# Performance work log

Measured on AMD Instinct MI355X. Metric: run time of the kernel, lower is better.

## Reference

```python
import jax, jax.numpy as jnp
import numpy as np

B, L, D_MODEL = 2, 2048, 1024
N_HEADS, D_K = 16, 64  # d_v == d_k (required by the output*q epilogue)


def setup_inputs() -> dict:
    key = jax.random.key(0)
    ks = jax.random.split(key, 8)
    # xavier_normal std for [d_model, d_k] fan: sqrt(2/(d_model+d_k))
    std = float(np.sqrt(2.0 / (D_MODEL + D_K)))
    std_p = float(np.sqrt(1.0 / (N_HEADS * D_K)))  # nn.Linear default ~ U(-1/sqrt(fan_in),..); normal approx ok for a baseline
    return {
        "q": jax.random.normal(ks[0], (B, L, D_MODEL), jnp.float32),
        "k": jax.random.normal(ks[1], (B, L, D_MODEL), jnp.float32),
        "v": jax.random.normal(ks[2], (B, L, D_MODEL), jnp.float32),
        "w_qs": jax.random.normal(ks[3], (N_HEADS, D_MODEL, D_K), jnp.float32) * std,
        "w_ks": jax.random.normal(ks[4], (N_HEADS, D_MODEL, D_K), jnp.float32) * std,
        "w_vs": jax.random.normal(ks[5], (N_HEADS, D_MODEL, D_K), jnp.float32) * std,
        "w_proj": jax.random.normal(ks[6], (D_MODEL, N_HEADS * D_K), jnp.float32) * std_p,
        "b_proj": jnp.zeros((D_MODEL,), jnp.float32),
    }


def reference(q, k, v, w_qs, w_ks, w_vs, w_proj, b_proj):
    # Per-head projections: [h, B, L, d_k]
    qh = jnp.einsum("bld,hdk->hblk", q, w_qs)
    kh = jnp.einsum("bld,hdk->hblk", k, w_ks)
    vh = jnp.einsum("bld,hdk->hblk", v, w_vs)
    # UNscaled attention (no 1/sqrt(d_k)), dropout is identity at eval
    attn = jax.nn.softmax(jnp.einsum("hblk,hbmk->hblm", qh, kh), axis=-1)
    # attn @ V with elementwise *q epilogue
    out = jnp.einsum("hblm,hbmk->hblk", attn, vh) * qh
    # torch.cat(torch.split(outputs, mb_size, 0), -1): heads concat on last dim
    out = out.transpose(1, 2, 0, 3).reshape(q.shape[0], q.shape[1], -1)  # [B, L, h*d_k]
    return out @ w_proj.T + b_proj
```

## Files before the change

### kernel.cpp

```cpp
#include <hip/hip_runtime.h>

#define B_ 2
#define L_ 2048
#define DM 1024
#define H_ 16
#define DK 64
#define ROWS (B_*L_)
#define BK 32
#define LDT 40

typedef _Float16 f16x8 __attribute__((ext_vector_type(8)));
typedef float    f32x4 __attribute__((ext_vector_type(4)));
typedef unsigned short us8 __attribute__((ext_vector_type(8)));
typedef unsigned short us4v __attribute__((ext_vector_type(4)));

__device__ __forceinline__ unsigned short f2h(float f) {
    _Float16 h = (_Float16)f;
    return __builtin_bit_cast(unsigned short, h);
}
__device__ __forceinline__ float h2f(unsigned short u) {
    return (float)__builtin_bit_cast(_Float16, u);
}
__device__ __forceinline__ f16x8 ld8h(const unsigned short* p) {
    return *reinterpret_cast<const f16x8*>(p);
}
__device__ __forceinline__ us8 cvt_us8(float4 a, float4 b) {
    us8 u;
    u[0] = f2h(a.x); u[1] = f2h(a.y); u[2] = f2h(a.z); u[3] = f2h(a.w);
    u[4] = f2h(b.x); u[5] = f2h(b.y); u[6] = f2h(b.z); u[7] = f2h(b.w);
    return u;
}

#define MFMA(a, b, c) __builtin_amdgcn_mfma_f32_16x16x32_f16((a), (b), (c), 0, 0, 0)

#define AS1 __attribute__((address_space(1)))
#define AS3 __attribute__((address_space(3)))
__device__ __forceinline__ void glds16(const void* g, void* l) {
    __builtin_amdgcn_global_load_lds((const AS1 unsigned int*)g,
                                     (AS3 unsigned int*)l, 16, 0, 0);
}

__global__ __launch_bounds__(256) void kcvt(
    const float* __restrict__ src, unsigned short* __restrict__ dst)
{
    size_t i = ((size_t)blockIdx.x * 256 + threadIdx.x) * 8;
    const float4* s4 = (const float4*)(src + i);
    *(us8*)(dst + i) = cvt_us8(s4[0], s4[1]);
}

__global__ __launch_bounds__(256) void kcvt3(
    const float* __restrict__ q, const float* __restrict__ k,
    const float* __restrict__ v, unsigned short* __restrict__ dst)
{
    int bx = blockIdx.x;
    int which = bx >> 11, rem = bx & 2047;
    const float* src = (which == 0) ? q : (which == 1) ? k : v;
    size_t i = ((size_t)rem * 256 + threadIdx.x) * 8;
    const float4* s4 = (const float4*)(src + i);
    *(us8*)(dst + (size_t)which * ROWS * DM + i) = cvt_us8(s4[0], s4[1]);
}

__global__ __launch_bounds__(256) void k0_transpose_w(
    const float* __restrict__ wq,
    const float* __restrict__ wk,
    const float* __restrict__ wv,
    unsigned short* __restrict__ wt)
{
    __shared__ unsigned short tile[64][65];
    int bx = blockIdx.x;
    int which = bx / (H_ * 16);
    int rem   = bx % (H_ * 16);
    int h  = rem >> 4;
    int db = (rem & 15) * 64;
    const float* src = (which == 0) ? wq : (which == 1) ? wk : wv;
    float scale = (which == 1) ? 1.44269504f : 1.0f;

    int t = threadIdx.x;
    int r = t >> 2;
    int c = (t & 3) * 16;
    const float4* sp = (const float4*)(src + ((size_t)(h * DM + db + r)) * DK + c);
    #pragma unroll
    for (int i4 = 0; i4 < 4; i4++) {
        float4 f = sp[i4];
        tile[r][c + i4 * 4 + 0] = f2h(f.x * scale);
        tile[r][c + i4 * 4 + 1] = f2h(f.y * scale);
        tile[r][c + i4 * 4 + 2] = f2h(f.z * scale);
        tile[r][c + i4 * 4 + 3] = f2h(f.w * scale);
    }
    __syncthreads();

    int n   = t >> 2;
    int d16 = (t & 3) * 16;
    __align__(16) unsigned short ov[16];
    #pragma unroll
    for (int i = 0; i < 16; i++) ov[i] = tile[d16 + i][n];
    size_t off = (((size_t)which * H_ + h) * DK + n) * DM + db + d16;
    *(us8*)(wt + off)     = *(us8*)&ov[0];
    *(us8*)(wt + off + 8) = *(us8*)&ov[8];
}

__global__ __launch_bounds__(256) void k1_proj_fp16(
    const unsigned short* __restrict__ qkvh,
    const unsigned short* __restrict__ wt,
    unsigned short* __restrict__ qh,
    unsigned short* __restrict__ kh,
    unsigned short* __restrict__ vt)
{
    __shared__ __align__(16) unsigned short sA[128 * BK];
    __shared__ __align__(16) unsigned short sB[128 * BK];

    int bx = blockIdx.x;
    int which = bx >> 8;
    int rem   = bx & 255;
    int mbase = (rem >> 3) * 128;
    int nbase = (rem & 7) * 128;

    const unsigned short* Ag = qkvh + (size_t)which * ROWS * DM;
    const unsigned short* Bg = wt + (size_t)which * DM * DM;

    int t = threadIdx.x;
    int wave = t >> 6, lane = t & 63, quad = lane >> 4, l16 = lane & 15;
    int wm = (wave >> 1) * 64, wn = (wave & 1) * 64;

    const unsigned short* gA0 = Ag + (size_t)(mbase + (t >> 2)) * DM + (t & 3) * 8;
    const unsigned short* gA1 = gA0 + (size_t)64 * DM;
    const unsigned short* gB0 = Bg + (size_t)(nbase + (t >> 2)) * DM + (t & 3) * 8;
    const unsigned short* gB1 = gB0 + (size_t)64 * DM;
    unsigned short* lA0 = &sA[(size_t)t * 8];
    unsigned short* lA1 = &sA[(size_t)(256 + t) * 8];
    unsigned short* lB0 = &sB[(size_t)t * 8];
    unsigned short* lB1 = &sB[(size_t)(256 + t) * 8];

    f32x4 acc[4][4];
    #pragma unroll
    for (int mi = 0; mi < 4; mi++)
        #pragma unroll
        for (int ni = 0; ni < 4; ni++) acc[mi][ni] = (f32x4)0.0f;

    for (int step = 0; step < 32; step++) {
        if (step) __syncthreads();
        glds16(gA0, lA0); glds16(gA1, lA1);
        glds16(gB0, lB0); glds16(gB1, lB1);
        gA0 += BK; gA1 += BK; gB0 += BK; gB1 += BK;
        __syncthreads();

        f16x8 aF[4], bF[4];
        #pragma unroll
        for (int mi = 0; mi < 4; mi++)
            aF[mi] = *(const f16x8*)&sA[(wm + mi * 16 + l16) * BK + quad * 8];
        #pragma unroll
        for (int ni = 0; ni < 4; ni++)
            bF[ni] = *(const f16x8*)&sB[(wn + ni * 16 + l16) * BK + quad * 8];
        __builtin_amdgcn_s_setprio(1);
        #pragma unroll
        for (int mi = 0; mi < 4; mi++)
            #pragma unroll
            for (int ni = 0; ni < 4; ni++)
                acc[mi][ni] = MFMA(aF[mi], bF[ni], acc[mi][ni]);
        __builtin_amdgcn_s_setprio(0);
    }

    int h = (nbase >> 6) + (wave & 1);
    if (which < 2) {
        unsigned short* OUT = ((which == 0) ? qh : kh) + (size_t)h * ROWS * DK;
        #pragma unroll
        for (int mi = 0; mi < 4; mi++)
            #pragma unroll
            for (int ni = 0; ni < 4; ni++)
                #pragma unroll
                for (int r = 0; r < 4; r++) {
                    int row = mbase + wm + mi * 16 + quad * 4 + r;
                    OUT[(size_t)row * DK + ni * 16 + l16] = f2h(acc[mi][ni][r]);
                }
    } else {
        unsigned short* OUT = vt + (size_t)h * DK * ROWS;
        #pragma unroll
        for (int mi = 0; mi < 4; mi++)
            #pragma unroll
            for (int ni = 0; ni < 4; ni++) {
                int dk   = ni * 16 + l16;
                int rowb = mbase + wm + mi * 16 + quad * 4;
                us4v pk;
                pk[0] = f2h(acc[mi][ni][0]); pk[1] = f2h(acc[mi][ni][1]);
                pk[2] = f2h(acc[mi][ni][2]); pk[3] = f2h(acc[mi][ni][3]);
                *(us4v*)(OUT + (size_t)dk * ROWS + rowb) = pk;
            }
    }
}

__global__ __launch_bounds__(256) void k1_proj_qkv(
    const float* __restrict__ q,
    const float* __restrict__ k,
    const float* __restrict__ v,
    const unsigned short* __restrict__ wt,
    unsigned short* __restrict__ qh,
    unsigned short* __restrict__ kh,
    unsigned short* __restrict__ vt)
{
    __shared__ __align__(16) unsigned short sA[128 * LDT];
    __shared__ __align__(16) unsigned short sB[128 * LDT];

    int bx = blockIdx.x;
    int which = bx >> 8;
    int rem   = bx & 255;
    int mbase = (rem >> 3) * 128;
    int nbase = (rem & 7) * 128;

    const float* Ag = (which == 0) ? q : (which == 1) ? k : v;
    const unsigned short* Bg = wt + (size_t)which * DM * DM;

    int t = threadIdx.x;
    int wave = t >> 6, lane = t & 63, quad = lane >> 4, l16 = lane & 15;
    int wm = (wave >> 1) * 64, wn = (wave & 1) * 64;

    int ar0 = t >> 2,         ac0 = t & 3;
    int ar1 = (256 + t) >> 2, ac1 = t & 3;
    const float* pA0 = Ag + (size_t)(mbase + ar0) * DM + ac0 * 8;
    const float* pA1 = Ag + (size_t)(mbase + ar1) * DM + ac1 * 8;
    const unsigned short* pB0 = Bg + (size_t)(nbase + ar0) * DM + ac0 * 8;
    const unsigned short* pB1 = Bg + (size_t)(nbase + ar1) * DM + ac1 * 8;
    unsigned short* wA0 = &sA[ar0 * LDT + ac0 * 8];
    unsigned short* wA1 = &sA[ar1 * LDT + ac1 * 8];
    unsigned short* wB0 = &sB[ar0 * LDT + ac0 * 8];
    unsigned short* wB1 = &sB[ar1 * LDT + ac1 * 8];

    f32x4 acc[4][4];
    #pragma unroll
    for (int mi = 0; mi < 4; mi++)
        #pragma unroll
        for (int ni = 0; ni < 4; ni++) acc[mi][ni] = (f32x4)0.0f;

    float4 rA0a = *(const float4*)pA0, rA0b = *(const float4*)(pA0 + 4);
    float4 rA1a = *(const float4*)pA1, rA1b = *(const float4*)(pA1 + 4);
    us8 rB0 = *(const us8*)pB0, rB1 = *(const us8*)pB1;

    for (int step = 0; step < 32; step++) {
        if (step) __syncthreads();
        *(us8*)wA0 = cvt_us8(rA0a, rA0b);
        *(us8*)wA1 = cvt_us8(rA1a, rA1b);
        *(us8*)wB0 = rB0; *(us8*)wB1 = rB1;
        __syncthreads();
        if (step < 31) {
            pA0 += BK; pA1 += BK; pB0 += BK; pB1 += BK;
            rA0a = *(const float4*)pA0; rA0b = *(const float4*)(pA0 + 4);
            rA1a = *(const float4*)pA1; rA1b = *(const float4*)(pA1 + 4);
            rB0 = *(const us8*)pB0; rB1 = *(const us8*)pB1;
        }
        f16x8 aF[4], bF[4];
        #pragma unroll
        for (int mi = 0; mi < 4; mi++)
            aF[mi] = *(const f16x8*)&sA[(wm + mi * 16 + l16) * LDT + quad * 8];
        #pragma unroll
        for (int ni = 0; ni < 4; ni++)
            bF[ni] = *(const f16x8*)&sB[(wn + ni * 16 + l16) * LDT + quad * 8];
        #pragma unroll
        for (int mi = 0; mi < 4; mi++)
            #pragma unroll
            for (int ni = 0; ni < 4; ni++)
                acc[mi][ni] = MFMA(aF[mi], bF[ni], acc[mi][ni]);
    }

    int h = (nbase >> 6) + (wave & 1);
    if (which < 2) {
        unsigned short* OUT = ((which == 0) ? qh : kh) + (size_t)h * ROWS * DK;
        #pragma unroll
        for (int mi = 0; mi < 4; mi++)
            #pragma unroll
            for (int ni = 0; ni < 4; ni++)
                #pragma unroll
                for (int r = 0; r < 4; r++) {
                    int row = mbase + wm + mi * 16 + quad * 4 + r;
                    OUT[(size_t)row * DK + ni * 16 + l16] = f2h(acc[mi][ni][r]);
                }
    } else {
        unsigned short* OUT = vt + (size_t)h * DK * ROWS;
        #pragma unroll
        for (int mi = 0; mi < 4; mi++)
            #pragma unroll
            for (int ni = 0; ni < 4; ni++) {
                int dk   = ni * 16 + l16;
                int rowb = mbase + wm + mi * 16 + quad * 4;
                us4v pk;
                pk[0] = f2h(acc[mi][ni][0]); pk[1] = f2h(acc[mi][ni][1]);
                pk[2] = f2h(acc[mi][ni][2]); pk[3] = f2h(acc[mi][ni][3]);
                *(us4v*)(OUT + (size_t)dk * ROWS + rowb) = pk;
            }
    }
}

__global__ __launch_bounds__(256) void k2_attn(
    const unsigned short* __restrict__ qh,
    const unsigned short* __restrict__ kh,
    const unsigned short* __restrict__ vt,
    unsigned short* __restrict__ x2)
{
    __shared__ __align__(16) unsigned short ktile[2][64][64];
    __shared__ __align__(16) unsigned short vtile[2][64][64];
    __shared__ __align__(16) unsigned short pld[4][16][64];

    int bx = blockIdx.x;
    int xcd = bx & 7;
    int loc = bx >> 3;
    int hb  = xcd * 4 + (loc >> 5);
    int qt  = loc & 31;
    int h = hb >> 1, b = hb & 1;
    int qbase = qt * 64;

    const unsigned short* qhp = qh + ((size_t)h * ROWS + b * L_) * DK;
    const unsigned short* khp = kh + ((size_t)h * ROWS + b * L_) * DK;
    const unsigned short* vtp = vt + (size_t)h * DK * ROWS + b * L_;

    int wave = threadIdx.x >> 6, lane = threadIdx.x & 63;
    int quad = lane >> 4, l16 = lane & 15;
    int t = threadIdx.x;
    int g8 = (l16 & 7) * 8;

    int c0 = t,       key0 = c0 >> 3, ss0 = ((c0 & 7) ^ (key0 & 7)) * 8;
    int c1 = 256 + t, key1 = c1 >> 3, ss1 = ((c1 & 7) ^ (key1 & 7)) * 8;
    const unsigned short* kg0 = khp + (size_t)key0 * DK + ss0;
    const unsigned short* kg1 = khp + (size_t)key1 * DK + ss1;
    const unsigned short* vg0 = vtp + (size_t)key0 * ROWS + ss0;
    const unsigned short* vg1 = vtp + (size_t)key1 * ROWS + ss1;
    unsigned short* kl0[2] = { &ktile[0][0][0] + c0 * 8, &ktile[1][0][0] + c0 * 8 };
    unsigned short* kl1[2] = { &ktile[0][0][0] + c1 * 8, &ktile[1][0][0] + c1 * 8 };
    unsigned short* vl0[2] = { &vtile[0][0][0] + c0 * 8, &vtile[1][0][0] + c0 * 8 };
    unsigned short* vl1[2] = { &vtile[0][0][0] + c1 * 8, &vtile[1][0][0] + c1 * 8 };

    const unsigned short* kgp0 = kg0 + (size_t)2 * 64 * DK;
    const unsigned short* kgp1 = kg1 + (size_t)2 * 64 * DK;
    const unsigned short* vgp0 = vg0 + 64;
    const unsigned short* vgp1 = vg1 + 64;

    glds16(kg0, kl0[0]); glds16(kg1, kl1[0]);
    glds16(kg0 + (size_t)64 * DK, kl0[1]); glds16(kg1 + (size_t)64 * DK, kl1[1]);
    glds16(vg0, vl0[0]); glds16(vg1, vl1[0]);

    int qrow = qbase + wave * 16 + l16;
    f16x8 qb0 = ld8h(qhp + (size_t)qrow * DK + quad * 8);
    f16x8 qb1 = ld8h(qhp + (size_t)qrow * DK + 32 + quad * 8);

    float m_i = -1e30f, l_i = 0.0f;
    f32x4 o[4];
    #pragma unroll
    for (int nt = 0; nt < 4; nt++) o[nt] = (f32x4)0.0f;

    f32x4 s0[4], s1[4];

    __syncthreads();

    #pragma unroll
    for (int nt = 0; nt < 4; nt++) s0[nt] = (f32x4)0.0f;
    __builtin_amdgcn_s_setprio(1);
    #pragma unroll
    for (int nt = 0; nt < 4; nt++) {
        const unsigned short* kr = &ktile[0][nt * 16 + l16][0];
        f16x8 ka0 = *(const f16x8*)(kr + ((quad * 8) ^ g8));
        f16x8 ka1 = *(const f16x8*)(kr + ((32 + quad * 8) ^ g8));
        s0[nt] = MFMA(ka0, qb0, s0[nt]);
        s0[nt] = MFMA(ka1, qb1, s0[nt]);
    }
    __builtin_amdgcn_s_setprio(0);
    __syncthreads();

#define K2_BODY(SP, SN, KT, CUR)                                              \
    {                                                                         \
        if ((KT) < 31) {                                                      \
            _Pragma("unroll")                                                 \
            for (int nt = 0; nt < 4; nt++) SN[nt] = (f32x4)0.0f;              \
            __builtin_amdgcn_s_setprio(1);                                    \
            _Pragma("unroll")                                                 \
            for (int nt = 0; nt < 4; nt++) {                                  \
                const unsigned short* kr = &ktile[(CUR)^1][nt * 16 + l16][0]; \
                f16x8 ka0 = *(const f16x8*)(kr + ((quad * 8) ^ g8));          \
                f16x8 ka1 = *(const f16x8*)(kr + ((32 + quad * 8) ^ g8));     \
                SN[nt] = MFMA(ka0, qb0, SN[nt]);                              \
                SN[nt] = MFMA(ka1, qb1, SN[nt]);                              \
            }                                                                 \
            __builtin_amdgcn_s_setprio(0);                                    \
        }                                                                     \
        if ((KT) < 30) {                                                      \
            glds16(kgp0, kl0[CUR]); glds16(kgp1, kl1[CUR]);                   \
            kgp0 += (size_t)64 * DK; kgp1 += (size_t)64 * DK;                 \
        }                                                                     \
        if ((KT) < 31) {                                                      \
            glds16(vgp0, vl0[(CUR)^1]); glds16(vgp1, vl1[(CUR)^1]);           \
            vgp0 += 64; vgp1 += 64;                                           \
        }                                                                     \
                                                 \
        float pm[4];                                                          \
        _Pragma("unroll")                                                     \
        for (int nt = 0; nt < 4; nt++) {                                      \
            float a = fmaxf(SP[nt][0], SP[nt][1]);                            \
            float c2 = fmaxf(SP[nt][2], SP[nt][3]);                           \
            pm[nt] = fmaxf(a, c2);                                            \
        }                                                                     \
        float mx = fmaxf(fmaxf(pm[0], pm[1]), fmaxf(pm[2], pm[3]));           \
        mx = fmaxf(mx, __shfl_xor(mx, 16));                                   \
        mx = fmaxf(mx, __shfl_xor(mx, 32));                                   \
        if (!__all(mx - m_i <= 11.0f)) {                                      \
            float mnew  = fmaxf(m_i, mx);                                     \
            float alpha = __builtin_amdgcn_exp2f(m_i - mnew);                 \
            l_i *= alpha;                                                     \
            _Pragma("unroll")                                                 \
            for (int r = 0; r < 4; r++) {                                     \
                float av = __shfl(alpha, quad * 4 + r);                       \
                _Pragma("unroll")                                             \
                for (int nt = 0; nt < 4; nt++) o[nt][r] *= av;                \
            }                                                                 \
            m_i = mnew;                                                       \
        }                                                                     \
        float ps[4];                                                          \
        _Pragma("unroll")                                                     \
        for (int nt = 0; nt < 4; nt++) {                                      \
            float e0 = __builtin_amdgcn_exp2f(SP[nt][0] - m_i);               \
            float e1 = __builtin_amdgcn_exp2f(SP[nt][1] - m_i);               \
            float e2 = __builtin_amdgcn_exp2f(SP[nt][2] - m_i);               \
            float e3 = __builtin_amdgcn_exp2f(SP[nt][3] - m_i);               \
            SP[nt][0] = e0; SP[nt][1] = e1; SP[nt][2] = e2; SP[nt][3] = e3;   \
            ps[nt] = (e0 + e1) + (e2 + e3);                                   \
        }                                                                     \
        float rs = (ps[0] + ps[1]) + (ps[2] + ps[3]);                         \
        rs += __shfl_xor(rs, 16);                                             \
        rs += __shfl_xor(rs, 32);                                             \
        l_i += rs;                                                            \
        _Pragma("unroll")                                                     \
        for (int nt = 0; nt < 4; nt++) {                                      \
            us4v pk;                                                          \
            pk[0] = f2h(SP[nt][0]); pk[1] = f2h(SP[nt][1]);                   \
            pk[2] = f2h(SP[nt][2]); pk[3] = f2h(SP[nt][3]);                   \
            *(us4v*)&pld[wave][l16][(nt * 16 + quad * 4) ^ g8] = pk;          \
        }                                                                     \
                                                      \
        __builtin_amdgcn_s_setprio(1);                                        \
        _Pragma("unroll")                                                     \
        for (int kk = 0; kk < 2; kk++) {                                      \
            f16x8 pa = *(const f16x8*)&pld[wave][l16][(kk*32 + quad*8) ^ g8]; \
            _Pragma("unroll")                                                 \
            for (int nt = 0; nt < 4; nt++) {                                  \
                const unsigned short* vr = &vtile[CUR][nt * 16 + l16][0];     \
                f16x8 vb = *(const f16x8*)(vr + ((kk * 32 + quad * 8) ^ g8)); \
                o[nt] = MFMA(pa, vb, o[nt]);                                  \
            }                                                                 \
        }                                                                     \
        __builtin_amdgcn_s_setprio(0);                                        \
        __syncthreads();                                                      \
    }

    for (int kt = 0; kt < 32; kt += 2) {
        K2_BODY(s0, s1, kt,     0)
        K2_BODY(s1, s0, kt + 1, 1)
    }
#undef K2_BODY

    float linv = 1.0f / l_i;
    #pragma unroll
    for (int r = 0; r < 4; r++) {
        float lv = __shfl(linv, quad * 4 + r);
        int row = qbase + wave * 16 + quad * 4 + r;
        #pragma unroll
        for (int nt = 0; nt < 4; nt++) {
            int col = nt * 16 + l16;
            float qv = h2f(qhp[(size_t)row * DK + col]);
            float val = o[nt][r] * lv * qv;
            x2[((size_t)b * L_ + row) * DM + h * DK + col] = f2h(val);
        }
    }
}

__global__ __launch_bounds__(256) void k3_out_proj(
    const unsigned short* __restrict__ x2,
    const unsigned short* __restrict__ wph,
    const float* __restrict__ bias,
    float* __restrict__ out)
{
    __shared__ __align__(16) unsigned short sA[128 * BK];
    __shared__ __align__(16) unsigned short sB[128 * BK];

    int bx = blockIdx.x;
    int mbase = (bx >> 3) * 128;
    int nbase = (bx & 7) * 128;

    int t = threadIdx.x;
    int wave = t >> 6, lane = t & 63, quad = lane >> 4, l16 = lane & 15;
    int wm = (wave >> 1) * 64, wn = (wave & 1) * 64;

    const unsigned short* gA0 = x2 + (size_t)(mbase + (t >> 2)) * DM + (t & 3) * 8;
    const unsigned short* gA1 = gA0 + (size_t)64 * DM;
    const unsigned short* gB0 = wph + (size_t)(nbase + (t >> 2)) * DM + (t & 3) * 8;
    const unsigned short* gB1 = gB0 + (size_t)64 * DM;
    unsigned short* lA0 = &sA[(size_t)t * 8];
    unsigned short* lA1 = &sA[(size_t)(256 + t) * 8];
    unsigned short* lB0 = &sB[(size_t)t * 8];
    unsigned short* lB1 = &sB[(size_t)(256 + t) * 8];

    f32x4 acc[4][4];
    #pragma unroll
    for (int mi = 0; mi < 4; mi++)
        #pragma unroll
        for (int ni = 0; ni < 4; ni++) acc[mi][ni] = (f32x4)0.0f;

    for (int step = 0; step < 32; step++) {
        if (step) __syncthreads();
        glds16(gA0, lA0); glds16(gA1, lA1);
        glds16(gB0, lB0); glds16(gB1, lB1);
        gA0 += BK; gA1 += BK; gB0 += BK; gB1 += BK;
        __syncthreads();

        f16x8 aF[4], bF[4];
        #pragma unroll
        for (int mi = 0; mi < 4; mi++)
            aF[mi] = *(const f16x8*)&sA[(wm + mi * 16 + l16) * BK + quad * 8];
        #pragma unroll
        for (int ni = 0; ni < 4; ni++)
            bF[ni] = *(const f16x8*)&sB[(wn + ni * 16 + l16) * BK + quad * 8];
        __builtin_amdgcn_s_setprio(1);
        #pragma unroll
        for (int mi = 0; mi < 4; mi++)
            #pragma unroll
            for (int ni = 0; ni < 4; ni++)
                acc[mi][ni] = MFMA(aF[mi], bF[ni], acc[mi][ni]);
        __builtin_amdgcn_s_setprio(0);
    }

    float bv[4];
    #pragma unroll
    for (int ni = 0; ni < 4; ni++) bv[ni] = bias[nbase + wn + ni * 16 + l16];

    #pragma unroll
    for (int mi = 0; mi < 4; mi++)
        #pragma unroll
        for (int ni = 0; ni < 4; ni++)
            #pragma unroll
            for (int r = 0; r < 4; r++) {
                int row = mbase + wm + mi * 16 + quad * 4 + r;
                int col = nbase + wn + ni * 16 + l16;
                out[(size_t)row * DM + col] = acc[mi][ni][r] + bv[ni];
            }
}

extern "C" void kernel_launch(void* const* d_in, const int* in_sizes, int n_in,
                              void* d_out, int out_size, void* d_ws, size_t ws_size,
                              hipStream_t stream)
{
    const float* q     = (const float*)d_in[0];
    const float* k     = (const float*)d_in[1];
    const float* v     = (const float*)d_in[2];
    const float* wqs   = (const float*)d_in[3];
    const float* wks   = (const float*)d_in[4];
    const float* wvs   = (const float*)d_in[5];
    const float* wproj = (const float*)d_in[6];
    const float* bproj = (const float*)d_in[7];
    float* out = (float*)d_out;

    char* ws = (char*)d_ws;
    #define MB (size_t)(1024 * 1024)
    unsigned short* wt   = (unsigned short*)(ws);
    unsigned short* wph  = (unsigned short*)(ws + 6  * MB);
    unsigned short* qh   = (unsigned short*)(ws + 8  * MB);
    unsigned short* kh   = (unsigned short*)(ws + 16 * MB);
    unsigned short* vt   = (unsigned short*)(ws + 24 * MB);
    unsigned short* x2   = (unsigned short*)(ws + 32 * MB);
    unsigned short* qkvh = (unsigned short*)(ws + 32 * MB);

    kcvt<<<dim3((DM * DM) / (256 * 8)), dim3(256), 0, stream>>>(wproj, wph);
    k0_transpose_w<<<dim3(3 * H_ * 16), dim3(256), 0, stream>>>(wqs, wks, wvs, wt);

    if (ws_size >= 56 * MB) {
        kcvt3<<<dim3(3 * 2048), dim3(256), 0, stream>>>(q, k, v, qkvh);
        k1_proj_fp16<<<dim3(3 * 32 * 8), dim3(256), 0, stream>>>(qkvh, wt, qh, kh, vt);
    } else {
        k1_proj_qkv<<<dim3(3 * 32 * 8), dim3(256), 0, stream>>>(q, k, v, wt, qh, kh, vt);
    }
    k2_attn<<<dim3(H_ * B_ * 32), dim3(256), 0, stream>>>(qh, kh, vt, x2);
    k3_out_proj<<<dim3(32 * 8), dim3(256), 0, stream>>>(x2, wph, bproj, out);
}
```

Measured before the change: 254.8 us.

## Fuse weight prep kernels, remap GEMM block order, simplify attention K pipeline

Merges the wproj conversion and QKV weight transpose into one launch to save a kernel launch. Remaps block indices in the projection and output GEMMs so consecutive workgroups land on different XCDs, aiming at better L2 locality. The fallback projection kernel now loads B through direct-to-LDS copies and raises wave priority around its MFMAs. The attention loop drops the software-pipelined QK^T (computing S for the next tile early) in favour of a simpler single-stage step with prefetch of K/V one tile ahead, and uses packed RTZ conversion for P; this trades overlap for lower register pressure and slightly different rounding.

```diff
diff --git a/kernel.cpp b/kernel.cpp
--- a/kernel.cpp
+++ b/kernel.cpp
@@ -10,6 +10,8 @@
 #define LDT 40
 
 typedef _Float16 f16x8 __attribute__((ext_vector_type(8)));
+typedef __fp16   fp16v2 __attribute__((ext_vector_type(2)));
+typedef __fp16   fp16v4 __attribute__((ext_vector_type(4)));
 typedef float    f32x4 __attribute__((ext_vector_type(4)));
 typedef unsigned short us8 __attribute__((ext_vector_type(8)));
 typedef unsigned short us4v __attribute__((ext_vector_type(4)));
@@ -40,12 +42,51 @@
                                      (AS3 unsigned int*)l, 16, 0, 0);
 }
 
-__global__ __launch_bounds__(256) void kcvt(
-    const float* __restrict__ src, unsigned short* __restrict__ dst)
-{
-    size_t i = ((size_t)blockIdx.x * 256 + threadIdx.x) * 8;
-    const float4* s4 = (const float4*)(src + i);
-    *(us8*)(dst + i) = cvt_us8(s4[0], s4[1]);
+__global__ __launch_bounds__(256) void kprep(
+    const float* __restrict__ wproj, unsigned short* __restrict__ wph,
+    const float* __restrict__ wq,
+    const float* __restrict__ wk,
+    const float* __restrict__ wv,
+    unsigned short* __restrict__ wt)
+{
+    int bxg = blockIdx.x;
+    if (bxg < 512) {
+        size_t i = ((size_t)bxg * 256 + threadIdx.x) * 8;
+        const float4* s4 = (const float4*)(wproj + i);
+        *(us8*)(wph + i) = cvt_us8(s4[0], s4[1]);
+        return;
+    }
+    __shared__ unsigned short tile[64][65];
+    int bx = bxg - 512;
+    int which = bx / (H_ * 16);
+    int rem   = bx % (H_ * 16);
+    int h  = rem >> 4;
+    int db = (rem & 15) * 64;
+    const float* src = (which == 0) ? wq : (which == 1) ? wk : wv;
+    float scale = (which == 1) ? 1.44269504f : 1.0f;
+
+    int t = threadIdx.x;
+    int r = t >> 2;
+    int c = (t & 3) * 16;
+    const float4* sp = (const float4*)(src + ((size_t)(h * DM + db + r)) * DK + c);
+    #pragma unroll
+    for (int i4 = 0; i4 < 4; i4++) {
+        float4 f = sp[i4];
+        tile[r][c + i4 * 4 + 0] = f2h(f.x * scale);
+        tile[r][c + i4 * 4 + 1] = f2h(f.y * scale);
+        tile[r][c + i4 * 4 + 2] = f2h(f.z * scale);
+        tile[r][c + i4 * 4 + 3] = f2h(f.w * scale);
+    }
+    __syncthreads();
+
+    int n   = t >> 2;
+    int d16 = (t & 3) * 16;
+    __align__(16) unsigned short ov[16];
+    #pragma unroll
+    for (int i = 0; i < 16; i++) ov[i] = tile[d16 + i][n];
+    size_t off = (((size_t)which * H_ + h) * DK + n) * DM + db + d16;
+    *(us8*)(wt + off)     = *(us8*)&ov[0];
+    *(us8*)(wt + off + 8) = *(us8*)&ov[8];
 }
 
 __global__ __launch_bounds__(256) void kcvt3(
@@ -60,45 +101,6 @@
     *(us8*)(dst + (size_t)which * ROWS * DM + i) = cvt_us8(s4[0], s4[1]);
 }
 
-__global__ __launch_bounds__(256) void k0_transpose_w(
-    const float* __restrict__ wq,
-    const float* __restrict__ wk,
-    const float* __restrict__ wv,
-    unsigned short* __restrict__ wt)
-{
-    __shared__ unsigned short tile[64][65];
-    int bx = blockIdx.x;
-    int which = bx / (H_ * 16);
-    int rem   = bx % (H_ * 16);
-    int h  = rem >> 4;
-    int db = (rem & 15) * 64;
-    const float* src = (which == 0) ? wq : (which == 1) ? wk : wv;
-    float scale = (which == 1) ? 1.44269504f : 1.0f;
-
-    int t = threadIdx.x;
-    int r = t >> 2;
-    int c = (t & 3) * 16;
-    const float4* sp = (const float4*)(src + ((size_t)(h * DM + db + r)) * DK + c);
-    #pragma unroll
-    for (int i4 = 0; i4 < 4; i4++) {
-        float4 f = sp[i4];
-        tile[r][c + i4 * 4 + 0] = f2h(f.x * scale);
-        tile[r][c + i4 * 4 + 1] = f2h(f.y * scale);
-        tile[r][c + i4 * 4 + 2] = f2h(f.z * scale);
-        tile[r][c + i4 * 4 + 3] = f2h(f.w * scale);
-    }
-    __syncthreads();
-
-    int n   = t >> 2;
-    int d16 = (t & 3) * 16;
-    __align__(16) unsigned short ov[16];
-    #pragma unroll
-    for (int i = 0; i < 16; i++) ov[i] = tile[d16 + i][n];
-    size_t off = (((size_t)which * H_ + h) * DK + n) * DM + db + d16;
-    *(us8*)(wt + off)     = *(us8*)&ov[0];
-    *(us8*)(wt + off + 8) = *(us8*)&ov[8];
-}
-
 __global__ __launch_bounds__(256) void k1_proj_fp16(
     const unsigned short* __restrict__ qkvh,
     const unsigned short* __restrict__ wt,
@@ -109,7 +111,8 @@
     __shared__ __align__(16) unsigned short sA[128 * BK];
     __shared__ __align__(16) unsigned short sB[128 * BK];
 
-    int bx = blockIdx.x;
+    int bxr = blockIdx.x;
+    int bx  = (bxr & 7) * 96 + (bxr >> 3);
     int which = bx >> 8;
     int rem   = bx & 255;
     int mbase = (rem >> 3) * 128;
@@ -198,9 +201,10 @@
     unsigned short* __restrict__ vt)
 {
     __shared__ __align__(16) unsigned short sA[128 * LDT];
-    __shared__ __align__(16) unsigned short sB[128 * LDT];
-
-    int bx = blockIdx.x;
+    __shared__ __align__(16) unsigned short sB[128 * BK];
+
+    int bxr = blockIdx.x;
+    int bx  = (bxr & 7) * 96 + (bxr >> 3);
     int which = bx >> 8;
     int rem   = bx & 255;
     int mbase = (rem >> 3) * 128;
@@ -217,12 +221,12 @@
     int ar1 = (256 + t) >> 2, ac1 = t & 3;
     const float* pA0 = Ag + (size_t)(mbase + ar0) * DM + ac0 * 8;
     const float* pA1 = Ag + (size_t)(mbase + ar1) * DM + ac1 * 8;
-    const unsigned short* pB0 = Bg + (size_t)(nbase + ar0) * DM + ac0 * 8;
-    const unsigned short* pB1 = Bg + (size_t)(nbase + ar1) * DM + ac1 * 8;
+    const unsigned short* gB0 = Bg + (size_t)(nbase + (t >> 2)) * DM + (t & 3) * 8;
+    const unsigned short* gB1 = gB0 + (size_t)64 * DM;
     unsigned short* wA0 = &sA[ar0 * LDT + ac0 * 8];
     unsigned short* wA1 = &sA[ar1 * LDT + ac1 * 8];
-    unsigned short* wB0 = &sB[ar0 * LDT + ac0 * 8];
-    unsigned short* wB1 = &sB[ar1 * LDT + ac1 * 8];
+    unsigned short* lB0 = &sB[(size_t)t * 8];
+    unsigned short* lB1 = &sB[(size_t)(256 + t) * 8];
 
     f32x4 acc[4][4];
     #pragma unroll
@@ -232,19 +236,18 @@
 
     float4 rA0a = *(const float4*)pA0, rA0b = *(const float4*)(pA0 + 4);
     float4 rA1a = *(const float4*)pA1, rA1b = *(const float4*)(pA1 + 4);
-    us8 rB0 = *(const us8*)pB0, rB1 = *(const us8*)pB1;
 
     for (int step = 0; step < 32; step++) {
         if (step) __syncthreads();
         *(us8*)wA0 = cvt_us8(rA0a, rA0b);
         *(us8*)wA1 = cvt_us8(rA1a, rA1b);
-        *(us8*)wB0 = rB0; *(us8*)wB1 = rB1;
+        glds16(gB0, lB0); glds16(gB1, lB1);
+        gB0 += BK; gB1 += BK;
         __syncthreads();
         if (step < 31) {
-            pA0 += BK; pA1 += BK; pB0 += BK; pB1 += BK;
+            pA0 += BK; pA1 += BK;
             rA0a = *(const float4*)pA0; rA0b = *(const float4*)(pA0 + 4);
             rA1a = *(const float4*)pA1; rA1b = *(const float4*)(pA1 + 4);
-            rB0 = *(const us8*)pB0; rB1 = *(const us8*)pB1;
         }
         f16x8 aF[4], bF[4];
         #pragma unroll
@@ -252,12 +255,14 @@
             aF[mi] = *(const f16x8*)&sA[(wm + mi * 16 + l16) * LDT + quad * 8];
         #pragma unroll
         for (int ni = 0; ni < 4; ni++)
-            bF[ni] = *(const f16x8*)&sB[(wn + ni * 16 + l16) * LDT + quad * 8];
+            bF[ni] = *(const f16x8*)&sB[(wn + ni * 16 + l16) * BK + quad * 8];
+        __builtin_amdgcn_s_setprio(1);
         #pragma unroll
         for (int mi = 0; mi < 4; mi++)
             #pragma unroll
             for (int ni = 0; ni < 4; ni++)
                 acc[mi][ni] = MFMA(aF[mi], bF[ni], acc[mi][ni]);
+        __builtin_amdgcn_s_setprio(0);
     }
 
     int h = (nbase >> 6) + (wave & 1);
@@ -326,13 +331,7 @@
     unsigned short* vl0[2] = { &vtile[0][0][0] + c0 * 8, &vtile[1][0][0] + c0 * 8 };
     unsigned short* vl1[2] = { &vtile[0][0][0] + c1 * 8, &vtile[1][0][0] + c1 * 8 };
 
-    const unsigned short* kgp0 = kg0 + (size_t)2 * 64 * DK;
-    const unsigned short* kgp1 = kg1 + (size_t)2 * 64 * DK;
-    const unsigned short* vgp0 = vg0 + 64;
-    const unsigned short* vgp1 = vg1 + 64;
-
     glds16(kg0, kl0[0]); glds16(kg1, kl1[0]);
-    glds16(kg0 + (size_t)64 * DK, kl0[1]); glds16(kg1 + (size_t)64 * DK, kl1[1]);
     glds16(vg0, vl0[0]); glds16(vg1, vl1[0]);
 
     int qrow = qbase + wave * 16 + l16;
@@ -344,54 +343,34 @@
     #pragma unroll
     for (int nt = 0; nt < 4; nt++) o[nt] = (f32x4)0.0f;
 
-    f32x4 s0[4], s1[4];
-
     __syncthreads();
 
-    #pragma unroll
-    for (int nt = 0; nt < 4; nt++) s0[nt] = (f32x4)0.0f;
-    __builtin_amdgcn_s_setprio(1);
-    #pragma unroll
-    for (int nt = 0; nt < 4; nt++) {
-        const unsigned short* kr = &ktile[0][nt * 16 + l16][0];
-        f16x8 ka0 = *(const f16x8*)(kr + ((quad * 8) ^ g8));
-        f16x8 ka1 = *(const f16x8*)(kr + ((32 + quad * 8) ^ g8));
-        s0[nt] = MFMA(ka0, qb0, s0[nt]);
-        s0[nt] = MFMA(ka1, qb1, s0[nt]);
-    }
-    __builtin_amdgcn_s_setprio(0);
-    __syncthreads();
-
-#define K2_BODY(SP, SN, KT, CUR)                                              \
+#define K2_STEP(KT, CUR)                                                      \
     {                                                                         \
         if ((KT) < 31) {                                                      \
-            _Pragma("unroll")                                                 \
-            for (int nt = 0; nt < 4; nt++) SN[nt] = (f32x4)0.0f;              \
-            __builtin_amdgcn_s_setprio(1);                                    \
-            _Pragma("unroll")                                                 \
-            for (int nt = 0; nt < 4; nt++) {                                  \
-                const unsigned short* kr = &ktile[(CUR)^1][nt * 16 + l16][0]; \
-                f16x8 ka0 = *(const f16x8*)(kr + ((quad * 8) ^ g8));          \
-                f16x8 ka1 = *(const f16x8*)(kr + ((32 + quad * 8) ^ g8));     \
-                SN[nt] = MFMA(ka0, qb0, SN[nt]);                              \
-                SN[nt] = MFMA(ka1, qb1, SN[nt]);                              \
-            }                                                                 \
-            __builtin_amdgcn_s_setprio(0);                                    \
-        }                                                                     \
-        if ((KT) < 30) {                                                      \
-            glds16(kgp0, kl0[CUR]); glds16(kgp1, kl1[CUR]);                   \
-            kgp0 += (size_t)64 * DK; kgp1 += (size_t)64 * DK;                 \
-        }                                                                     \
-        if ((KT) < 31) {                                                      \
-            glds16(vgp0, vl0[(CUR)^1]); glds16(vgp1, vl1[(CUR)^1]);           \
-            vgp0 += 64; vgp1 += 64;                                           \
-        }                                                                     \
-                                                 \
+            size_t ko = (size_t)((KT) + 1) * 64 * DK;                         \
+            size_t vo = (size_t)((KT) + 1) * 64;                              \
+            glds16(kg0 + ko, kl0[(CUR) ^ 1]); glds16(kg1 + ko, kl1[(CUR) ^ 1]);\
+            glds16(vg0 + vo, vl0[(CUR) ^ 1]); glds16(vg1 + vo, vl1[(CUR) ^ 1]);\
+        }                                                                     \
+        f32x4 s[4];                                                           \
+        _Pragma("unroll")                                                     \
+        for (int nt = 0; nt < 4; nt++) s[nt] = (f32x4)0.0f;                   \
+        __builtin_amdgcn_s_setprio(1);                                        \
+        _Pragma("unroll")                                                     \
+        for (int nt = 0; nt < 4; nt++) {                                      \
+            const unsigned short* kr = &ktile[CUR][nt * 16 + l16][0];         \
+            f16x8 ka0 = *(const f16x8*)(kr + ((quad * 8) ^ g8));              \
+            f16x8 ka1 = *(const f16x8*)(kr + ((32 + quad * 8) ^ g8));         \
+            s[nt] = MFMA(ka0, qb0, s[nt]);                                    \
+            s[nt] = MFMA(ka1, qb1, s[nt]);                                    \
+        }                                                                     \
+        __builtin_amdgcn_s_setprio(0);                                        \
         float pm[4];                                                          \
         _Pragma("unroll")                                                     \
         for (int nt = 0; nt < 4; nt++) {                                      \
-            float a = fmaxf(SP[nt][0], SP[nt][1]);                            \
-            float c2 = fmaxf(SP[nt][2], SP[nt][3]);                           \
+            float a = fmaxf(s[nt][0], s[nt][1]);                              \
+            float c2 = fmaxf(s[nt][2], s[nt][3]);                             \
             pm[nt] = fmaxf(a, c2);                                            \
         }                                                                     \
         float mx = fmaxf(fmaxf(pm[0], pm[1]), fmaxf(pm[2], pm[3]));           \
@@ -412,11 +391,11 @@
         float ps[4];                                                          \
         _Pragma("unroll")                                                     \
         for (int nt = 0; nt < 4; nt++) {                                      \
-            float e0 = __builtin_amdgcn_exp2f(SP[nt][0] - m_i);               \
-            float e1 = __builtin_amdgcn_exp2f(SP[nt][1] - m_i);               \
-            float e2 = __builtin_amdgcn_exp2f(SP[nt][2] - m_i);               \
-            float e3 = __builtin_amdgcn_exp2f(SP[nt][3] - m_i);               \
-            SP[nt][0] = e0; SP[nt][1] = e1; SP[nt][2] = e2; SP[nt][3] = e3;   \
+            float e0 = __builtin_amdgcn_exp2f(s[nt][0] - m_i);                \
+            float e1 = __builtin_amdgcn_exp2f(s[nt][1] - m_i);                \
+            float e2 = __builtin_amdgcn_exp2f(s[nt][2] - m_i);                \
+            float e3 = __builtin_amdgcn_exp2f(s[nt][3] - m_i);                \
+            s[nt][0] = e0; s[nt][1] = e1; s[nt][2] = e2; s[nt][3] = e3;       \
             ps[nt] = (e0 + e1) + (e2 + e3);                                   \
         }                                                                     \
         float rs = (ps[0] + ps[1]) + (ps[2] + ps[3]);                         \
@@ -425,16 +404,15 @@
         l_i += rs;                                                            \
         _Pragma("unroll")                                                     \
         for (int nt = 0; nt < 4; nt++) {                                      \
-            us4v pk;                                                          \
-            pk[0] = f2h(SP[nt][0]); pk[1] = f2h(SP[nt][1]);                   \
-            pk[2] = f2h(SP[nt][2]); pk[3] = f2h(SP[nt][3]);                   \
-            *(us4v*)&pld[wave][l16][(nt * 16 + quad * 4) ^ g8] = pk;          \
-        }                                                                     \
-                                                      \
+            fp16v2 p01 = __builtin_amdgcn_cvt_pkrtz(s[nt][0], s[nt][1]);      \
+            fp16v2 p23 = __builtin_amdgcn_cvt_pkrtz(s[nt][2], s[nt][3]);      \
+            fp16v4 pk4 = __builtin_shufflevector(p01, p23, 0, 1, 2, 3);       \
+            *(fp16v4*)&pld[wave][l16][(nt * 16 + quad * 4) ^ g8] = pk4;       \
+        }                                                                     \
         __builtin_amdgcn_s_setprio(1);                                        \
         _Pragma("unroll")                                                     \
         for (int kk = 0; kk < 2; kk++) {                                      \
-            f16x8 pa = *(const f16x8*)&pld[wave][l16][(kk*32 + quad*8) ^ g8]; \
+            f16x8 pa = *(const f16x8*)&pld[wave][l16][(kk * 32 + quad * 8) ^ g8];\
             _Pragma("unroll")                                                 \
             for (int nt = 0; nt < 4; nt++) {                                  \
                 const unsigned short* vr = &vtile[CUR][nt * 16 + l16][0];     \
@@ -446,11 +424,11 @@
         __syncthreads();                                                      \
     }
 
-    for (int kt = 0; kt < 32; kt += 2) {
-        K2_BODY(s0, s1, kt,     0)
-        K2_BODY(s1, s0, kt + 1, 1)
-    }
-#undef K2_BODY
+    for (int kt2 = 0; kt2 < 32; kt2 += 2) {
+        K2_STEP(kt2,     0)
+        K2_STEP(kt2 + 1, 1)
+    }
+#undef K2_STEP
 
     float linv = 1.0f / l_i;
     #pragma unroll
@@ -476,7 +454,8 @@
     __shared__ __align__(16) unsigned short sA[128 * BK];
     __shared__ __align__(16) unsigned short sB[128 * BK];
 
-    int bx = blockIdx.x;
+    int bxr = blockIdx.x;
+    int bx  = (bxr & 7) * 32 + (bxr >> 3);
     int mbase = (bx >> 3) * 128;
     int nbase = (bx & 7) * 128;
 
@@ -562,8 +541,8 @@
     unsigned short* x2   = (unsigned short*)(ws + 32 * MB);
     unsigned short* qkvh = (unsigned short*)(ws + 32 * MB);
 
-    kcvt<<<dim3((DM * DM) / (256 * 8)), dim3(256), 0, stream>>>(wproj, wph);
-    k0_transpose_w<<<dim3(3 * H_ * 16), dim3(256), 0, stream>>>(wqs, wks, wvs, wt);
+    kprep<<<dim3(512 + 3 * H_ * 16), dim3(256), 0, stream>>>(
+        wproj, wph, wqs, wks, wvs, wt);
 
     if (ws_size >= 56 * MB) {
         kcvt3<<<dim3(3 * 2048), dim3(256), 0, stream>>>(q, k, v, qkvh);
```

Result: faster. 231.9 us (-9.0%).
